# Optimization experiments

Hardware: AMD Instinct MI355X
Metric: run time of the kernel (lower is better)

The kernel has to match this reference:

```python
import jax, jax.numpy as jnp
import numpy as np

N = 8192            # number of ROIs
FEAT = 255          # num_classes(151) + embed_dim(100) + pos_dim(4)
HID = 64
PRE_NMS = 6000      # eval-mode pre_nms_topn
POST_NMS = 300      # eval-mode post_nms_topn
NMS_THRESH = 0.7


def setup_inputs() -> dict:
    key = jax.random.key(0)
    ks = jax.random.split(key, 12)
    # rois: [N,5] = (im_ind, x1, y1, x2, y2), valid boxes in a 1024x1024 image
    x1 = jax.random.uniform(ks[0], (N,)) * 900.0
    y1 = jax.random.uniform(ks[1], (N,)) * 900.0
    w = jax.random.uniform(ks[2], (N,)) * 120.0 + 4.0
    h = jax.random.uniform(ks[3], (N,)) * 120.0 + 4.0
    rois = jnp.stack([jnp.zeros((N,)), x1, y1, x1 + w, y1 + h], axis=1).astype(jnp.float32)
    roi_feat = jax.random.normal(ks[4], (N, FEAT), dtype=jnp.float32)
    s = 0.05
    return {
        "rois": rois,
        "roi_feat": roi_feat,
        "W_sub1": jax.random.normal(ks[5], (FEAT, HID), jnp.float32) * s,
        "b_sub1": jnp.zeros((HID,), jnp.float32),
        "W_sub2": jax.random.normal(ks[6], (HID, HID), jnp.float32) * s,
        "b_sub2": jnp.zeros((HID,), jnp.float32),
        "W_obj1": jax.random.normal(ks[7], (FEAT, HID), jnp.float32) * s,
        "b_obj1": jnp.zeros((HID,), jnp.float32),
        "W_obj2": jax.random.normal(ks[8], (HID, HID), jnp.float32) * s,
        "b_obj2": jnp.zeros((HID,), jnp.float32),
    }


def _iou_matrix(boxes):
    # boxes: [K,4] (x1,y1,x2,y2) -> [K,K] IoU
    x1, y1, x2, y2 = boxes[:, 0], boxes[:, 1], boxes[:, 2], boxes[:, 3]
    area = (x2 - x1) * (y2 - y1)
    ix1 = jnp.maximum(x1[:, None], x1[None, :])
    iy1 = jnp.maximum(y1[:, None], y1[None, :])
    ix2 = jnp.minimum(x2[:, None], x2[None, :])
    iy2 = jnp.minimum(y2[:, None], y2[None, :])
    inter = jnp.maximum(ix2 - ix1, 0.0) * jnp.maximum(iy2 - iy1, 0.0)
    return inter / (area[:, None] + area[None, :] - inter + 1e-8)


def reference(rois, roi_feat, W_sub1, b_sub1, W_sub2, b_sub2,
              W_obj1, b_obj1, W_obj2, b_obj2):
    # Original detaches roi_feat before the bilinear head.
    f = jax.lax.stop_gradient(roi_feat)
    x_sub = jnp.maximum(f @ W_sub1 + b_sub1, 0.0) @ W_sub2 + b_sub2  # [N,64]
    x_obj = jnp.maximum(f @ W_obj1 + b_obj1, 0.0) @ W_obj2 + b_obj2  # [N,64]
    scores = jax.nn.sigmoid(x_sub @ x_obj.T)                          # [N,N]

    n = scores.shape[0]
    # exclude self-pairs (sub == obj)
    diag = jnp.arange(n)
    flat = scores.at[diag, diag].set(-1.0).reshape(-1)

    # pre-NMS top-k over all N*N pairs (sorted descending)
    top_s, top_i = jax.lax.top_k(flat, PRE_NMS)
    sub = top_i // n
    obj = top_i % n

    boxes = jax.lax.stop_gradient(rois[:, 1:5])
    bs, bo = boxes[sub], boxes[obj]
    # union box of each (sub,obj) pair for relation NMS
    union = jnp.concatenate([jnp.minimum(bs[:, :2], bo[:, :2]),
                             jnp.maximum(bs[:, 2:], bo[:, 2:])], axis=1)  # [PRE,4]
    iou = _iou_matrix(union)                                              # [PRE,PRE]
    # non-greedy (matrix) NMS: suppress i if any higher-ranked j overlaps > thresh
    higher = jnp.triu(jnp.ones((PRE_NMS, PRE_NMS), bool), k=1)  # [j,i] true when j < i
    suppressed = jnp.any((iou > NMS_THRESH) & higher, axis=0)
    kept_scores = jnp.where(suppressed, -1.0, top_s)

    post_s, post_k = jax.lax.top_k(kept_scores, POST_NMS)
    rel_inds = jnp.stack([sub[post_k], obj[post_k]], axis=1)  # [POST,2]
    return rel_inds, post_s
```

## Files before the change

kernel.cpp:

```cpp
#include <hip/hip_runtime.h>
#include <math.h>

#define NB    8192
#define FEAT  255
#define HID   64
#define TOPK  6000
#define POSTK 300
#define BINS  8192
#define BSHIFT 19
#define CAP   131072
#define CAPLIM 16384
#define SLACK 1
#define TSEL  500
#define SAMPF 16
#define JSLICES 128
#define LCAP  2048
#define NMS_ICH 64

typedef __attribute__((ext_vector_type(8))) short bf16x8;
typedef __attribute__((ext_vector_type(4))) float f32x4;
typedef __attribute__((ext_vector_type(4))) double f64x4;

__device__ __forceinline__ unsigned binOf(float x) {
    unsigned u = __float_as_uint(x);
    u = (u & 0x80000000u) ? ~u : (u | 0x80000000u);
    return u >> BSHIFT;
}

__device__ __forceinline__ unsigned short f2bf(float f) {
    unsigned u = __float_as_uint(f);
    return (unsigned short)((u + 0x7fffu + ((u >> 16) & 1u)) >> 16);
}

__global__ __launch_bounds__(256) void mlp_kernel(
    const float* __restrict__ feat,
    const float* __restrict__ W1s, const float* __restrict__ b1s,
    const float* __restrict__ W2s, const float* __restrict__ b2s,
    const float* __restrict__ W1o, const float* __restrict__ b1o,
    const float* __restrict__ W2o, const float* __restrict__ b2o,
    double* __restrict__ Xs64, double* __restrict__ Xo64,
    unsigned short* __restrict__ Xsb, unsigned short* __restrict__ Xob)
{
    __shared__ float  fl[16 * 258];
    __shared__ double hl[16][65];

    int tid  = threadIdx.x;
    int lane = tid & 63;
    int w    = tid >> 6;
    int a16  = lane & 15;
    int kq   = lane >> 4;
    int bx   = blockIdx.x;
    int net  = bx & 1;
    int rbase = (bx >> 1) * 16;
    int c0   = w * 16 + a16;

    const float* fsrc = feat + (size_t)rbase * FEAT;
    for (int idx = tid; idx < 16 * FEAT; idx += 256) {
        int r = idx / FEAT;
        int k = idx - r * FEAT;
        fl[r * 258 + k] = fsrc[idx];
    }
    if (tid < 16) fl[tid * 258 + 255] = 0.0f;
    __syncthreads();

    const float* W1 = net ? W1o : W1s;
    const float* B1 = net ? b1o : b1s;
    const float* W2 = net ? W2o : W2s;
    const float* B2 = net ? b2o : b2s;
    double*       X  = net ? Xo64 : Xs64;
    unsigned short* Xb = net ? Xob : Xsb;

    f64x4 acc0 = {0, 0, 0, 0};
#pragma unroll 4
    for (int ks = 0; ks < 63; ++ks) {
        int k = ks * 4 + kq;
        double av = (double)fl[a16 * 258 + k];
        double b0 = (double)W1[k * HID + c0];
        acc0 = __builtin_amdgcn_mfma_f64_16x16x4f64(av, b0, acc0, 0, 0, 0);
    }
    {
        int k = 252 + kq;
        double av = (double)fl[a16 * 258 + k];
        double b0 = 0.0;
        if (k < FEAT) b0 = (double)W1[k * HID + c0];
        acc0 = __builtin_amdgcn_mfma_f64_16x16x4f64(av, b0, acc0, 0, 0, 0);
    }

    {
        double bb0 = (double)B1[c0];
#pragma unroll
        for (int i = 0; i < 4; ++i) {
            int r = kq * 4 + i;
            double v0 = acc0[i] + bb0;
            hl[r][c0] = v0 > 0.0 ? v0 : 0.0;
        }
    }
    __syncthreads();

    f64x4 x0 = {0, 0, 0, 0};
#pragma unroll 4
    for (int ks = 0; ks < 16; ++ks) {
        int k = ks * 4 + kq;
        double av = hl[a16][k];
        double b0 = (double)W2[k * HID + c0];
        x0 = __builtin_amdgcn_mfma_f64_16x16x4f64(av, b0, x0, 0, 0, 0);
    }

    {
        double bb0 = (double)B2[c0];
#pragma unroll
        for (int i = 0; i < 4; ++i) {
            int r = kq * 4 + i;
            double v0 = x0[i] + bb0;
            size_t o0 = (size_t)(rbase + r) * HID + c0;
            X[o0] = v0;
            Xb[o0] = f2bf((float)v0);
        }
    }
}

__global__ __launch_bounds__(256) void mfma_hist(
    const unsigned short* __restrict__ Xsb, const unsigned short* __restrict__ Xob,
    unsigned* __restrict__ ghist, unsigned* __restrict__ ctrl)
{
    __shared__ unsigned hist[BINS];
    __shared__ unsigned csum[256];
    __shared__ bool win_s;
    int tid = threadIdx.x;
    for (int i = tid; i < BINS; i += 256) hist[i] = 0u;
    __syncthreads();

    int lane = tid & 63;
    int wave = tid >> 6;
    int quad = lane >> 4;
    int l16  = lane & 15;
    int r0 = blockIdx.y * 128 + (wave >> 1) * 64;
    int c0 = blockIdx.x * 128 + (wave & 1) * 64;

    f32x4 acc[4][4];
    bf16x8 afr[2][4], bfr[2][4];
#pragma unroll
    for (int kc = 0; kc < 2; ++kc)
#pragma unroll
        for (int t = 0; t < 4; ++t) {
            afr[kc][t] = *(const bf16x8*)(Xsb + (size_t)(r0 + t * 16 + l16) * HID + kc * 32 + quad * 8);
            bfr[kc][t] = *(const bf16x8*)(Xob + (size_t)(c0 + t * 16 + l16) * HID + kc * 32 + quad * 8);
        }
#pragma unroll
    for (int ti = 0; ti < 4; ++ti)
#pragma unroll
        for (int tj = 0; tj < 4; ++tj) acc[ti][tj] = (f32x4){0, 0, 0, 0};
#pragma unroll
    for (int kc = 0; kc < 2; ++kc)
#pragma unroll
        for (int ti = 0; ti < 4; ++ti)
#pragma unroll
            for (int tj = 0; tj < 4; ++tj)
                acc[ti][tj] = __builtin_amdgcn_mfma_f32_16x16x32_bf16(
                    afr[kc][ti], bfr[kc][tj], acc[ti][tj], 0, 0, 0);

#pragma unroll
    for (int ti = 0; ti < 4; ++ti)
#pragma unroll
        for (int tj = 0; tj < 4; ++tj)
#pragma unroll
            for (int i = 0; i < 4; ++i) {
                int r = r0 + ti * 16 + quad * 4 + i;
                int c = c0 + tj * 16 + l16;
                float v = acc[ti][tj][i];
                if (v > 0.0f && r != c)
                    atomicAdd(&hist[binOf(v)], 1u);
            }

    __syncthreads();
    for (int i = tid; i < BINS; i += 256) {
        unsigned h = hist[i];
        if (h) atomicAdd(&ghist[i], h);
    }

    __syncthreads();
    if (tid == 0) {
        __threadfence();
        unsigned done = atomicAdd(&ctrl[3], 1u);
        win_s = (done == gridDim.x * gridDim.y - 1u);
    }
    __syncthreads();
    if (!win_s) return;

    for (int i = tid; i < BINS; i += 256)
        hist[i] = __hip_atomic_load(&ghist[i], __ATOMIC_RELAXED, __HIP_MEMORY_SCOPE_AGENT);
    __syncthreads();

    int base = tid * (BINS / 256);
    unsigned s = 0;
    for (int i = 0; i < BINS / 256; ++i) s += hist[base + i];
    csum[tid] = s;
    __syncthreads();
    if (tid == 0) {
        unsigned run = 0;
        for (int c = 255; c >= 0; --c) { run += csum[c]; csum[c] = run; }
    }
    __syncthreads();

    unsigned above = (tid == 255) ? 0u : csum[tid + 1];
    unsigned prev = above;
    for (int b = base + BINS / 256 - 1; b >= base; --b) {
        unsigned cur = prev + hist[b];
        if (cur >= TSEL && prev < TSEL) {
            unsigned bstar = (unsigned)b;
            unsigned bt = bstar >= SLACK ? bstar - SLACK : 0;
            unsigned cnt = cur;
            for (unsigned bb = bstar; bb-- > bt;) cnt += hist[bb];
            while ((unsigned)SAMPF * cnt > CAPLIM && bt < bstar) { cnt -= hist[bt]; bt++; }
            ctrl[1] = bt;
            unsigned key = bt << BSHIFT;
            unsigned fbits;
            if (key == 0u) fbits = 0xff800000u;
            else fbits = (key & 0x80000000u) ? (key ^ 0x80000000u) : ~key;
            ctrl[2] = fbits;
            break;
        }
        prev = cur;
    }
}

__global__ __launch_bounds__(256) void mfma_filter(
    const unsigned short* __restrict__ Xsb, const unsigned short* __restrict__ Xob,
    unsigned* __restrict__ ctrl, unsigned* __restrict__ cidx)
{
    __shared__ unsigned lcnt;
    __shared__ unsigned gbase;
    __shared__ unsigned lbuf[LCAP];
    float vt = __uint_as_float(ctrl[2]);
    int tid = threadIdx.x;
    if (tid == 0) lcnt = 0;

    int lane = tid & 63;
    int wave = tid >> 6;
    int quad = lane >> 4;
    int l16  = lane & 15;
    int r0 = blockIdx.y * 128 + (wave >> 1) * 64;
    int cb = blockIdx.x * 256 + (wave & 1) * 64;

    bf16x8 afr[2][4];
#pragma unroll
    for (int kc = 0; kc < 2; ++kc)
#pragma unroll
        for (int t = 0; t < 4; ++t)
            afr[kc][t] = *(const bf16x8*)(Xsb + (size_t)(r0 + t * 16 + l16) * HID + kc * 32 + quad * 8);

    bf16x8 b0[2], b1[2];
    {
        int col0 = cb + l16;
        int col1 = cb + 16 + l16;
#pragma unroll
        for (int kc = 0; kc < 2; ++kc) {
            b0[kc] = *(const bf16x8*)(Xob + (size_t)col0 * HID + kc * 32 + quad * 8);
            b1[kc] = *(const bf16x8*)(Xob + (size_t)col1 * HID + kc * 32 + quad * 8);
        }
    }

    __syncthreads();

#pragma unroll
    for (int q = 0; q < 8; ++q) {
        int ct = q >> 2, tj = q & 3;
        int c0 = cb + ct * 128;
        int cj = c0 + tj * 16 + l16;
        bool nodiag = (r0 != c0);

        bf16x8 b2[2];
        if (q < 6) {
            int q2 = q + 2;
            int col2 = cb + (q2 >> 2) * 128 + (q2 & 3) * 16 + l16;
#pragma unroll
            for (int kc = 0; kc < 2; ++kc)
                b2[kc] = *(const bf16x8*)(Xob + (size_t)col2 * HID + kc * 32 + quad * 8);
        }

        f32x4 acc[4];
#pragma unroll
        for (int ti = 0; ti < 4; ++ti) acc[ti] = (f32x4){0, 0, 0, 0};
#pragma unroll
        for (int kc = 0; kc < 2; ++kc)
#pragma unroll
            for (int ti = 0; ti < 4; ++ti)
                acc[ti] = __builtin_amdgcn_mfma_f32_16x16x32_bf16(
                    afr[kc][ti], b0[kc], acc[ti], 0, 0, 0);

        unsigned hm = 0u;
#pragma unroll
        for (int ti = 0; ti < 4; ++ti)
#pragma unroll
            for (int i = 0; i < 4; ++i) {
                bool hit = acc[ti][i] >= vt;
                if (!nodiag) {
                    int r = r0 + ti * 16 + quad * 4 + i;
                    hit = hit && (r != cj);
                }
                hm |= hit ? (1u << (ti * 4 + i)) : 0u;
            }

        if (__any(hm != 0u)) {
#pragma unroll
            for (int ti = 0; ti < 4; ++ti)
#pragma unroll
                for (int i = 0; i < 4; ++i) {
                    if (hm & (1u << (ti * 4 + i))) {
                        int r = r0 + ti * 16 + quad * 4 + i;
                        unsigned rc = (unsigned)r * (unsigned)NB + (unsigned)cj;
                        unsigned p = atomicAdd(&lcnt, 1u);
                        if (p < LCAP) {
                            lbuf[p] = rc;
                        } else {
                            unsigned g = atomicAdd(&ctrl[0], 1u);
                            if (g < CAP) cidx[g] = rc;
                        }
                    }
                }
        }

        if (q < 6) {
            b0[0] = b1[0]; b0[1] = b1[1];
            b1[0] = b2[0]; b1[1] = b2[1];
        } else if (q == 6) {
            b0[0] = b1[0]; b0[1] = b1[1];
        }
    }

    __syncthreads();
    unsigned n = lcnt; if (n > LCAP) n = LCAP;
    if (tid == 0 && n) gbase = atomicAdd(&ctrl[0], n);
    __syncthreads();
    for (unsigned i = tid; i < n; i += 256u) {
        unsigned p = gbase + i;
        if (p < CAP) cidx[p] = lbuf[i];
    }
}

__global__ __launch_bounds__(256) void refine_kernel(
    const unsigned* __restrict__ ctrl, const unsigned* __restrict__ cidx,
    const double* __restrict__ Xs64, const double* __restrict__ Xo64,
    double* __restrict__ cval)
{
    unsigned M = ctrl[0];
    if (M > CAP) M = CAP;
    unsigned nw = gridDim.x * 4u;
    int lane = threadIdx.x & 63;
    for (unsigned w = blockIdx.x * 4u + (threadIdx.x >> 6); w < M; w += nw) {
        unsigned id = cidx[w];
        unsigned r = id >> 13, c = id & (NB - 1);
        double p = Xs64[(size_t)r * HID + lane] * Xo64[(size_t)c * HID + lane];
#pragma unroll
        for (int s = 32; s > 0; s >>= 1) p += __shfl_xor(p, s);
        if (lane == 0) cval[w] = (r == c) ? -1.0 : p;
    }
}

__global__ __launch_bounds__(256) void rank_count(
    const unsigned* __restrict__ ctrl,
    const double* __restrict__ cval, const unsigned* __restrict__ cidx,
    unsigned* __restrict__ rank)
{
    unsigned M = ctrl[0];
    if (M > CAP) M = CAP;

    unsigned slice = blockIdx.y;
    unsigned jbeg = (unsigned)(((unsigned long long)slice * M) / JSLICES);
    unsigned jend = (unsigned)(((unsigned long long)(slice + 1) * M) / JSLICES);

    __shared__ double  lv[256];
    __shared__ unsigned li[256];

    for (unsigned itile = blockIdx.x; itile * 1024u < M; itile += gridDim.x) {
        unsigned i0 = itile * 1024u + threadIdx.x;
        double v[4];
        unsigned id[4];
        unsigned cnt[4] = {0, 0, 0, 0};
#pragma unroll
        for (int k = 0; k < 4; ++k) {
            unsigned idx = i0 + (unsigned)k * 256u;
            bool a = idx < M;
            v[k]  = a ? cval[idx] : 0.0;
            id[k] = a ? cidx[idx] : 0u;
        }

        for (unsigned base = jbeg; base < jend; base += 256u) {
            unsigned j = base + threadIdx.x;
            if (j < jend) { lv[threadIdx.x] = cval[j]; li[threadIdx.x] = cidx[j]; }
            __syncthreads();
            unsigned lim = jend - base; if (lim > 256u) lim = 256u;
            for (unsigned e = 0; e < lim; ++e) {
                double ev = lv[e];
                unsigned ei = li[e];
#pragma unroll
                for (int k = 0; k < 4; ++k)
                    cnt[k] += (ev > v[k]) || (ev == v[k] && ei < id[k]);
            }
            __syncthreads();
        }
#pragma unroll
        for (int k = 0; k < 4; ++k) {
            unsigned idx = i0 + (unsigned)k * 256u;
            if (idx < M && cnt[k]) atomicAdd(&rank[idx], cnt[k]);
        }
    }
}

__global__ __launch_bounds__(256) void rank_scatter_prep(
    const unsigned* __restrict__ ctrl,
    const double* __restrict__ cval, const unsigned* __restrict__ cidx,
    const unsigned* __restrict__ rank, const float* __restrict__ rois,
    double* __restrict__ sval, unsigned* __restrict__ sidx,
    double* __restrict__ ub)
{
    unsigned M = ctrl[0];
    if (M > CAP) M = CAP;
    unsigned stride = gridDim.x * 256u;
    for (unsigned t = blockIdx.x * 256u + threadIdx.x; t < M; t += stride) {
        unsigned rk = rank[t];
        if (rk < TOPK) {
            unsigned id = cidx[t];
            sval[rk] = cval[t];
            sidx[rk] = id;
            unsigned s = id >> 13, o = id & (NB - 1);
            const float* bs = rois + (size_t)s * 5;
            const float* bo = rois + (size_t)o * 5;
            double x1 = fmin((double)bs[1], (double)bo[1]);
            double y1 = fmin((double)bs[2], (double)bo[2]);
            double x2 = fmax((double)bs[3], (double)bo[3]);
            double y2 = fmax((double)bs[4], (double)bo[4]);
            double area = (x2 - x1) * (y2 - y1);
            double* u = ub + (size_t)rk * 5;
            u[0] = x1; u[1] = y1; u[2] = x2; u[3] = y2; u[4] = 0.7 * area;
        }
    }
}

__global__ __launch_bounds__(256) void nms_kernel(
    const double* __restrict__ ub, unsigned* sup)
{
    int jb = blockIdx.x;
    int ic = blockIdx.y;
    int ibase = ic * NMS_ICH;
    if (ibase >= TOPK) return;
    if (ibase >= jb * 256 + 255) return;

    __shared__ double L[NMS_ICH][5];
    int tid = threadIdx.x;
    int icount = TOPK - ibase; if (icount > NMS_ICH) icount = NMS_ICH;
    for (int q = tid; q < icount * 5; q += 256)
        L[q / 5][q % 5] = ub[(size_t)ibase * 5 + q];
    __syncthreads();

    int j = jb * 256 + tid;
    if (j >= TOPK) return;
    int lim = j - ibase; if (lim > icount) lim = icount;
    if (lim <= 0) return;

    const double* u = ub + (size_t)j * 5;
    double x1 = u[0], y1 = u[1], x2 = u[2], y2 = u[3], pa = u[4];
    bool flag = false;
    for (int e = 0; e < lim; ++e) {
        double ix1 = fmax(L[e][0], x1);
        double iy1 = fmax(L[e][1], y1);
        double ix2 = fmin(L[e][2], x2);
        double iy2 = fmin(L[e][3], y2);
        double iw = ix2 - ix1; iw = iw > 0.0 ? iw : 0.0;
        double ih = iy2 - iy1; ih = ih > 0.0 ? ih : 0.0;
        flag |= (1.7 * (iw * ih) > pa + L[e][4] + 7e-9);
    }
    if (flag) sup[j] = 1u;
}

__global__ __launch_bounds__(1024) void finalize_kernel(
    const unsigned* __restrict__ sup, const double* __restrict__ sval,
    const unsigned* __restrict__ sidx, float* __restrict__ out)
{
    __shared__ unsigned wsum[16];
    __shared__ unsigned red2[16][2];
    __shared__ unsigned totalu_s, ubase_s;
    int tid  = threadIdx.x;
    int lane = tid & 63;
    int w    = tid >> 6;
    int mybase = blockIdx.x * 1024;

    unsigned tot = 0, bef = 0;
    for (int i = tid; i < TOPK; i += 1024) {
        unsigned f = (sup[i] == 0u) ? 1u : 0u;
        tot += f;
        bef += (i < mybase) ? f : 0u;
    }
#pragma unroll
    for (int st = 32; st > 0; st >>= 1) {
        tot += __shfl_down(tot, st);
        bef += __shfl_down(bef, st);
    }
    if (lane == 0) { red2[w][0] = tot; red2[w][1] = bef; }
    __syncthreads();
    if (tid == 0) {
        unsigned t = 0, b = 0;
        for (int i = 0; i < 16; ++i) { t += red2[i][0]; b += red2[i][1]; }
        totalu_s = t; ubase_s = b;
    }
    __syncthreads();
    unsigned totalu = totalu_s;
    unsigned ubase  = ubase_s;
    unsigned sbase  = (unsigned)mybase - ubase;

    int idx = mybase + tid;
    unsigned f = (idx < TOPK && sup[idx] == 0u) ? 1u : 0u;
    unsigned long long m = __ballot(f != 0u);
    if (lane == 0) wsum[w] = (unsigned)__popcll(m);
    __syncthreads();
    unsigned wbase = 0;
#pragma unroll
    for (int i = 0; i < 16; ++i)
        if (i < w) wbase += wsum[i];
    unsigned e = wbase + (unsigned)__popcll(m & ((1ull << lane) - 1ull));
    if (idx < TOPK) {
        unsigned pos = f ? (ubase + e)
                         : (totalu + sbase + (unsigned)tid - e);
        if (pos < POSTK) {
            unsigned id = sidx[idx];
            unsigned sb = id >> 13, ob = id & (NB - 1);
            out[2 * pos]     = (float)sb;
            out[2 * pos + 1] = (float)ob;
            double sg = f ? 1.0 / (1.0 + exp(-sval[idx])) : -1.0;
            out[2 * POSTK + pos] = (float)sg;
        }
    }
}

extern "C" void kernel_launch(void* const* d_in, const int* in_sizes, int n_in,
                              void* d_out, int out_size, void* d_ws, size_t ws_size,
                              hipStream_t stream)
{
    const float* rois = (const float*)d_in[0];
    const float* feat = (const float*)d_in[1];
    const float* W1s  = (const float*)d_in[2];
    const float* b1s  = (const float*)d_in[3];
    const float* W2s  = (const float*)d_in[4];
    const float* b2s  = (const float*)d_in[5];
    const float* W1o  = (const float*)d_in[6];
    const float* b1o  = (const float*)d_in[7];
    const float* W2o  = (const float*)d_in[8];
    const float* b2o  = (const float*)d_in[9];

    char* ws = (char*)d_ws;
    size_t off = 0;
    auto alloc = [&](size_t bytes) -> void* {
        off = (off + 255) & ~(size_t)255;
        void* p = ws + off;
        off += bytes;
        return p;
    };

    unsigned* ghist = (unsigned*)alloc((size_t)BINS * 4);
    unsigned* ctrl  = (unsigned*)alloc(256);
    unsigned* sup   = (unsigned*)alloc((size_t)6144 * 4);
    unsigned* rank  = (unsigned*)alloc((size_t)CAP * 4);
    size_t zero_bytes = off;

    double* Xs64 = (double*)alloc((size_t)NB * HID * 8);
    double* Xo64 = (double*)alloc((size_t)NB * HID * 8);
    unsigned short* Xsb = (unsigned short*)alloc((size_t)NB * HID * 2);
    unsigned short* Xob = (unsigned short*)alloc((size_t)NB * HID * 2);
    double* cval = (double*)alloc((size_t)CAP * 8);
    unsigned* cidx = (unsigned*)alloc((size_t)CAP * 4);
    double* svalv = (double*)alloc((size_t)TOPK * 8);
    unsigned* sidxv = (unsigned*)alloc((size_t)TOPK * 4);
    double* ub   = (double*)alloc((size_t)TOPK * 5 * 8);

    (void)hipMemsetAsync(d_ws, 0, zero_bytes, stream);

    mlp_kernel<<<(NB / 16) * 2, 256, 0, stream>>>(feat, W1s, b1s, W2s, b2s,
                                                  W1o, b1o, W2o, b2o,
                                                  Xs64, Xo64, Xsb, Xob);
    mfma_hist<<<dim3(4, 64), 256, 0, stream>>>(Xsb, Xob, ghist, ctrl);
    mfma_filter<<<dim3(32, 64), 256, 0, stream>>>(Xsb, Xob, ctrl, cidx);
    refine_kernel<<<2048, 256, 0, stream>>>(ctrl, cidx, Xs64, Xo64, cval);
    rank_count<<<dim3(16, JSLICES), 256, 0, stream>>>(ctrl, cval, cidx, rank);
    rank_scatter_prep<<<512, 256, 0, stream>>>(ctrl, cval, cidx, rank, rois,
                                               svalv, sidxv, ub);
    nms_kernel<<<dim3((TOPK + 255) / 256, (TOPK + NMS_ICH - 1) / NMS_ICH), 256, 0, stream>>>(ub, sup);
    finalize_kernel<<<(TOPK + 1023) / 1024, 1024, 0, stream>>>(sup, svalv, sidxv, (float*)d_out);
}
```

Before: 217.3 us.

## Fuse fp64 candidate refinement into the filter kernel and drop rank memset

Removes the separate refine kernel: each filter block now computes the exact fp64 dot product for its locally buffered candidates right after reserving global slots, and zeroes the matching rank entries. The rank array is taken out of the memset region because every live slot is now initialised in the filter kernel. This saves one launch, one re-read of cidx, and a 512 KB memset, at the cost of longer filter blocks and a serial scalar overflow path. The diagonal self-pair is no longer forced to -1 here, but the filter's hit test already excludes r==c.

```diff
diff --git a/kernel.cpp b/kernel.cpp
--- a/kernel.cpp
+++ b/kernel.cpp
@@ -226,7 +226,9 @@
 
 __global__ __launch_bounds__(256) void mfma_filter(
     const unsigned short* __restrict__ Xsb, const unsigned short* __restrict__ Xob,
-    unsigned* __restrict__ ctrl, unsigned* __restrict__ cidx)
+    unsigned* __restrict__ ctrl, unsigned* __restrict__ cidx,
+    const double* __restrict__ Xs64, const double* __restrict__ Xo64,
+    double* __restrict__ cval, unsigned* __restrict__ rank)
 {
     __shared__ unsigned lcnt;
     __shared__ unsigned gbase;
@@ -314,7 +316,15 @@
                             lbuf[p] = rc;
                         } else {
                             unsigned g = atomicAdd(&ctrl[0], 1u);
-                            if (g < CAP) cidx[g] = rc;
+                            if (g < CAP) {
+                                cidx[g] = rc;
+                                const double* xr = Xs64 + (size_t)r * HID;
+                                const double* xc = Xo64 + (size_t)cj * HID;
+                                double a64 = 0.0;
+                                for (int k = 0; k < HID; ++k) a64 += xr[k] * xc[k];
+                                cval[g] = a64;
+                                rank[g] = 0u;
+                            }
                         }
                     }
                 }
@@ -336,24 +346,17 @@
         unsigned p = gbase + i;
         if (p < CAP) cidx[p] = lbuf[i];
     }
-}
-
-__global__ __launch_bounds__(256) void refine_kernel(
-    const unsigned* __restrict__ ctrl, const unsigned* __restrict__ cidx,
-    const double* __restrict__ Xs64, const double* __restrict__ Xo64,
-    double* __restrict__ cval)
-{
-    unsigned M = ctrl[0];
-    if (M > CAP) M = CAP;
-    unsigned nw = gridDim.x * 4u;
-    int lane = threadIdx.x & 63;
-    for (unsigned w = blockIdx.x * 4u + (threadIdx.x >> 6); w < M; w += nw) {
-        unsigned id = cidx[w];
-        unsigned r = id >> 13, c = id & (NB - 1);
-        double p = Xs64[(size_t)r * HID + lane] * Xo64[(size_t)c * HID + lane];
-#pragma unroll
-        for (int s = 32; s > 0; s >>= 1) p += __shfl_xor(p, s);
-        if (lane == 0) cval[w] = (r == c) ? -1.0 : p;
+
+    for (unsigned i = (unsigned)wave; i < n; i += 4u) {
+        unsigned g = gbase + i;
+        if (g < CAP) {
+            unsigned rc = lbuf[i];
+            unsigned r = rc >> 13, c = rc & (NB - 1u);
+            double pr = Xs64[(size_t)r * HID + lane] * Xo64[(size_t)c * HID + lane];
+#pragma unroll
+            for (int s = 32; s > 0; s >>= 1) pr += __shfl_xor(pr, s);
+            if (lane == 0) { cval[g] = pr; rank[g] = 0u; }
+        }
     }
 }
 
@@ -559,9 +562,9 @@
     unsigned* ghist = (unsigned*)alloc((size_t)BINS * 4);
     unsigned* ctrl  = (unsigned*)alloc(256);
     unsigned* sup   = (unsigned*)alloc((size_t)6144 * 4);
+    size_t zero_bytes = off;
+
     unsigned* rank  = (unsigned*)alloc((size_t)CAP * 4);
-    size_t zero_bytes = off;
-
     double* Xs64 = (double*)alloc((size_t)NB * HID * 8);
     double* Xo64 = (double*)alloc((size_t)NB * HID * 8);
     unsigned short* Xsb = (unsigned short*)alloc((size_t)NB * HID * 2);
@@ -578,8 +581,8 @@
                                                   W1o, b1o, W2o, b2o,
                                                   Xs64, Xo64, Xsb, Xob);
     mfma_hist<<<dim3(4, 64), 256, 0, stream>>>(Xsb, Xob, ghist, ctrl);
-    mfma_filter<<<dim3(32, 64), 256, 0, stream>>>(Xsb, Xob, ctrl, cidx);
-    refine_kernel<<<2048, 256, 0, stream>>>(ctrl, cidx, Xs64, Xo64, cval);
+    mfma_filter<<<dim3(32, 64), 256, 0, stream>>>(Xsb, Xob, ctrl, cidx,
+                                                  Xs64, Xo64, cval, rank);
     rank_count<<<dim3(16, JSLICES), 256, 0, stream>>>(ctrl, cval, cidx, rank);
     rank_scatter_prep<<<512, 256, 0, stream>>>(ctrl, cval, cidx, rank, rois,
                                                svalv, sidxv, ub);
```

Measured after the change: 229.7 us. 5.7% more time.
